# Performance work log

Hardware: AMD Instinct MI355X
Metric: run time of the kernel (lower is better)

## Reference

```python
import jax, jax.numpy as jnp
import numpy as np

N_NODES = 100000
N_EDGES = 6400000
D = 12

def setup_inputs() -> dict:
    key = jax.random.key(0)
    k1, k2, k3, k4 = jax.random.split(key, 4)
    x = jax.random.normal(k1, (N_NODES, D), dtype=jnp.float32)
    W_l = jax.random.normal(k2, (D, D), dtype=jnp.float32) / np.sqrt(D)
    W_r = jax.random.normal(k3, (D, D), dtype=jnp.float32) / np.sqrt(D)
    b = jnp.zeros((D,), dtype=jnp.float32)
    edge_index = jax.random.randint(k4, (2, N_EDGES), 0, N_NODES, dtype=jnp.int64)
    return {"x": x, "W_l": W_l, "W_r": W_r, "b": b, "edge_index": edge_index}

def reference(x, W_l, W_r, b, edge_index):
    # PyG SAGEConv (mean aggregation): out = lin_l(mean_{j in N(i)} x_j) + lin_r(x_i)
    src = edge_index[0]
    dst = edge_index[1]
    n = x.shape[0]
    msgs = x[src]                                      # [E, D] gather
    agg = jax.ops.segment_sum(msgs, dst, num_segments=n)          # [N, D]
    cnt = jax.ops.segment_sum(jnp.ones_like(dst, dtype=x.dtype), dst, num_segments=n)
    mean = agg / jnp.maximum(cnt, 1.0)[:, None]        # [N, D]
    out = mean @ W_l.T + x @ W_r.T + b                 # lin_l carries the bias in PyG
    return out
```

## Files before the change

kernel.cpp:

```cpp
#include <hip/hip_runtime.h>

#define N_NODES 100000
#define N_EDGES 6400000
#define D 12

#define SLOG 7
#define SSZ  128
#define NB   ((N_NODES + SSZ - 1) / SSZ)
#define NBLK 512
#define EPB  ((N_EDGES + NBLK - 1) / NBLK)
#define SBLK 256
#define STHR 512
#define SEPB ((N_EDGES + SBLK - 1) / SBLK)
#define RSTR 13

#define CAP  2048
#define EPT  (CAP / 256)

__device__ __forceinline__ unsigned int f2bf(float f) {
    unsigned int u = __float_as_uint(f);
    return (u + 0x7fffu + ((u >> 16) & 1u)) >> 16;
}
__device__ __forceinline__ unsigned int pk2(float lo, float hi) {
    return (f2bf(hi) << 16) | f2bf(lo);
}
__device__ __forceinline__ float bflo(unsigned int u) { return __uint_as_float(u << 16); }
__device__ __forceinline__ float bfhi(unsigned int u) { return __uint_as_float(u & 0xffff0000u); }

__global__ __launch_bounds__(256) void prep_kernel(
    const float* __restrict__ x, unsigned int* __restrict__ xb)
{
    int i = blockIdx.x * 256 + threadIdx.x;
    if (i >= N_NODES) return;
    const float4* xr = (const float4*)(x) + (size_t)i * 3;
    float4 a = xr[0], b = xr[1], c = xr[2];
    unsigned int* o = xb + (size_t)i * 8;
    ((uint4*)o)[0] = make_uint4(pk2(a.x, a.y), pk2(a.z, a.w), pk2(b.x, b.y), pk2(b.z, b.w));
    ((uint2*)(o + 4))[0] = make_uint2(pk2(c.x, c.y), pk2(c.z, c.w));
}

__global__ __launch_bounds__(256) void hist_kernel(
    const int* __restrict__ ei, int* __restrict__ bins)
{
    __shared__ int h[NB];
    for (int i = threadIdx.x; i < NB; i += 256) h[i] = 0;
    __syncthreads();
    const int* dei = ei + N_EDGES;
    int start = blockIdx.x * EPB;
    int end = min(start + EPB, N_EDGES);
    int e = start + (int)threadIdx.x;
    while (e + 768 < end) {
        int d0 = dei[e], d1 = dei[e + 256], d2 = dei[e + 512], d3 = dei[e + 768];
        atomicAdd(&h[d0 >> SLOG], 1);
        atomicAdd(&h[d1 >> SLOG], 1);
        atomicAdd(&h[d2 >> SLOG], 1);
        atomicAdd(&h[d3 >> SLOG], 1);
        e += 1024;
    }
    while (e < end) { atomicAdd(&h[dei[e] >> SLOG], 1); e += 256; }
    __syncthreads();
    for (int i = threadIdx.x; i < NB; i += 256) {
        int c = h[i];
        if (c) atomicAdd(&bins[i], c);
    }
}

__global__ __launch_bounds__(1024) void scan_kernel(
    const int* __restrict__ bins, int* __restrict__ base, int* __restrict__ cursor)
{
    __shared__ int buf[1024];
    __shared__ int carry;
    int tid = threadIdx.x;
    if (tid == 0) carry = 0;
    __syncthreads();
    for (int c0 = 0; c0 < NB; c0 += 1024) {
        int i = c0 + tid;
        int v = (i < NB) ? bins[i] : 0;
        buf[tid] = v;
        __syncthreads();
        for (int o = 1; o < 1024; o <<= 1) {
            int t = (tid >= o) ? buf[tid - o] : 0;
            __syncthreads();
            buf[tid] += t;
            __syncthreads();
        }
        int excl = buf[tid] - v + carry;
        if (i < NB) { base[i] = excl; cursor[i] = excl; }
        __syncthreads();
        if (tid == 0) carry += buf[1023];
        __syncthreads();
    }
    if (tid == 0) base[NB] = N_EDGES;
}

__global__ __launch_bounds__(512) void scatter_sort_kernel(
    const int* __restrict__ ei, int* __restrict__ cursor,
    unsigned int* __restrict__ sorted)
{
    __shared__ int h[NB];
    for (int i = threadIdx.x; i < NB; i += STHR) h[i] = 0;
    __syncthreads();
    const int* dei = ei + N_EDGES;
    int start = blockIdx.x * SEPB;
    int end = min(start + SEPB, N_EDGES);
    int e = start + (int)threadIdx.x;
    while (e + 3 * STHR < end) {
        int d0 = dei[e], d1 = dei[e + STHR], d2 = dei[e + 2 * STHR], d3 = dei[e + 3 * STHR];
        atomicAdd(&h[d0 >> SLOG], 1);
        atomicAdd(&h[d1 >> SLOG], 1);
        atomicAdd(&h[d2 >> SLOG], 1);
        atomicAdd(&h[d3 >> SLOG], 1);
        e += 4 * STHR;
    }
    while (e < end) { atomicAdd(&h[dei[e] >> SLOG], 1); e += STHR; }
    __syncthreads();
    for (int i = threadIdx.x; i < NB; i += STHR) {
        int c = h[i];
        h[i] = c ? atomicAdd(&cursor[i], c) : 0;
    }
    __syncthreads();
    e = start + (int)threadIdx.x;
    while (e + 3 * STHR < end) {
        int s0 = ei[e], s1 = ei[e + STHR], s2 = ei[e + 2 * STHR], s3 = ei[e + 3 * STHR];
        int d0 = dei[e], d1 = dei[e + STHR], d2 = dei[e + 2 * STHR], d3 = dei[e + 3 * STHR];
        int p0 = atomicAdd(&h[d0 >> SLOG], 1);
        int p1 = atomicAdd(&h[d1 >> SLOG], 1);
        int p2 = atomicAdd(&h[d2 >> SLOG], 1);
        int p3 = atomicAdd(&h[d3 >> SLOG], 1);
        sorted[p0] = ((unsigned)s0 << SLOG) | (unsigned)(d0 & (SSZ - 1));
        sorted[p1] = ((unsigned)s1 << SLOG) | (unsigned)(d1 & (SSZ - 1));
        sorted[p2] = ((unsigned)s2 << SLOG) | (unsigned)(d2 & (SSZ - 1));
        sorted[p3] = ((unsigned)s3 << SLOG) | (unsigned)(d3 & (SSZ - 1));
        e += 4 * STHR;
    }
    while (e < end) {
        int s = ei[e], d = dei[e];
        int pos = atomicAdd(&h[d >> SLOG], 1);
        sorted[pos] = ((unsigned)s << SLOG) | (unsigned)(d & (SSZ - 1));
        e += STHR;
    }
}

__global__ __launch_bounds__(256) void agg_reg_kernel(
    const unsigned int* __restrict__ sorted, const int* __restrict__ base,
    const unsigned int* __restrict__ xb,
    const float* __restrict__ x, const float* __restrict__ Wl,
    const float* __restrict__ Wr, const float* __restrict__ bias,
    float* __restrict__ out)
{
    __shared__ float sWl[D * D], sWr[D * D], sb[D];
    __shared__ int cnt[SSZ];
    __shared__ int sbuf[SSZ];
    __shared__ int segbase[SSZ + 1];
    __shared__ int cursor[SSZ];
    __shared__ int cnt_tot[SSZ];
    __shared__ unsigned vals[CAP * 6];

    int t = threadIdx.x;
    int b = blockIdx.x;

    if (t < D * D) { sWl[t] = Wl[t]; sWr[t] = Wr[t]; }
    if (t < D) sb[t] = bias[t];
    if (t < SSZ) cnt_tot[t] = 0;

    float acc[D];
#pragma unroll
    for (int d = 0; d < D; ++d) acc[d] = 0.f;

    int loc = t >> 1;
    int sub = t & 1;

    int start = base[b];
    int end = base[b + 1];

    for (int c0 = start; c0 < end; c0 += CAP) {
        int n = min(CAP, end - c0);
        if (t < SSZ) cnt[t] = 0;
        __syncthreads();

        unsigned pe[EPT];
        int ne = 0;
        for (int j = t; j < n; j += 256) pe[ne++] = sorted[c0 + j];
#pragma unroll
        for (int k = 0; k < EPT; ++k)
            if (k < ne) atomicAdd(&cnt[pe[k] & (SSZ - 1)], 1);
        __syncthreads();

        if (t < SSZ) sbuf[t] = cnt[t];
        __syncthreads();
        for (int o = 1; o < SSZ; o <<= 1) {
            int v = (t < SSZ && t >= o) ? sbuf[t - o] : 0;
            __syncthreads();
            if (t < SSZ) sbuf[t] += v;
            __syncthreads();
        }
        if (t < SSZ) {
            segbase[t + 1] = sbuf[t];
            if (t == 0) segbase[0] = 0;
        }
        __syncthreads();
        if (t < SSZ) { cursor[t] = segbase[t]; cnt_tot[t] += cnt[t]; }
        __syncthreads();

#pragma unroll
        for (int k = 0; k < EPT; ++k) {
            if (k < ne) {
                unsigned p = pe[k];
                int slot = atomicAdd(&cursor[p & (SSZ - 1)], 1);
                const unsigned* r = xb + (size_t)(p >> SLOG) * 8;
                uint2 q0 = ((const uint2*)r)[0];
                uint2 q1 = ((const uint2*)r)[1];
                uint2 q2 = ((const uint2*)r)[2];
                unsigned* vv = &vals[slot * 6];
                ((uint2*)vv)[0] = q0;
                ((uint2*)vv)[1] = q1;
                ((uint2*)vv)[2] = q2;
            }
        }
        __syncthreads();

        int s0 = segbase[loc], s1 = segbase[loc + 1];
        for (int j = s0 + sub; j < s1; j += 2) {
            const unsigned* vv = &vals[j * 6];
            uint2 q0 = ((const uint2*)vv)[0];
            uint2 q1 = ((const uint2*)vv)[1];
            uint2 q2 = ((const uint2*)vv)[2];
            acc[0]  += bflo(q0.x); acc[1]  += bfhi(q0.x);
            acc[2]  += bflo(q0.y); acc[3]  += bfhi(q0.y);
            acc[4]  += bflo(q1.x); acc[5]  += bfhi(q1.x);
            acc[6]  += bflo(q1.y); acc[7]  += bfhi(q1.y);
            acc[8]  += bflo(q2.x); acc[9]  += bfhi(q2.x);
            acc[10] += bflo(q2.y); acc[11] += bfhi(q2.y);
        }
        __syncthreads();
    }

    float* red = (float*)vals;
#pragma unroll
    for (int d = 0; d < D; ++d) red[sub * 1664 + loc * 13 + d] = acc[d];
    __syncthreads();

    if (t < SSZ) {
        int node = b * SSZ + t;
        if (node < N_NODES) {
            float m[D];
#pragma unroll
            for (int d = 0; d < D; ++d)
                m[d] = red[t * 13 + d] + red[1664 + t * 13 + d];
            float inv = 1.f / fmaxf((float)cnt_tot[t], 1.f);
#pragma unroll
            for (int d = 0; d < D; ++d) m[d] *= inv;

            float xi[D];
            const float4* xr = (const float4*)(x) + (size_t)node * 3;
            float4 x0 = xr[0], x1 = xr[1], x2 = xr[2];
            xi[0] = x0.x; xi[1] = x0.y; xi[2]  = x0.z; xi[3]  = x0.w;
            xi[4] = x1.x; xi[5] = x1.y; xi[6]  = x1.z; xi[7]  = x1.w;
            xi[8] = x2.x; xi[9] = x2.y; xi[10] = x2.z; xi[11] = x2.w;

            float o[D];
#pragma unroll
            for (int oo = 0; oo < D; ++oo) {
                float a = sb[oo];
#pragma unroll
                for (int d = 0; d < D; ++d) {
                    a += m[d] * sWl[oo * D + d];
                    a += xi[d] * sWr[oo * D + d];
                }
                o[oo] = a;
            }
            float4* orow = (float4*)(out) + (size_t)node * 3;
            orow[0] = make_float4(o[0], o[1], o[2], o[3]);
            orow[1] = make_float4(o[4], o[5], o[6], o[7]);
            orow[2] = make_float4(o[8], o[9], o[10], o[11]);
        }
    }
}

__global__ __launch_bounds__(256) void agg_finalize_f32_kernel(
    const unsigned int* __restrict__ sorted, const int* __restrict__ base,
    const float* __restrict__ x, const float* __restrict__ Wl,
    const float* __restrict__ Wr, const float* __restrict__ bias,
    float* __restrict__ out)
{
    __shared__ float agg[SSZ * RSTR];
    __shared__ float sWl[D * D], sWr[D * D], sb[D];
    int t = threadIdx.x;
    int b = blockIdx.x;
    for (int i = t; i < SSZ * RSTR; i += 256) agg[i] = 0.f;
    if (t < D * D) { sWl[t] = Wl[t]; sWr[t] = Wr[t]; }
    if (t < D) sb[t] = bias[t];
    __syncthreads();
    int start = base[b];
    int end = base[b + 1];
    for (int e = start + t; e < end; e += 256) {
        unsigned p = sorted[e];
        int src = (int)(p >> SLOG);
        int lc = (int)(p & (SSZ - 1));
        const float4* xr = (const float4*)(x) + (size_t)src * 3;
        float4 a = xr[0], b4 = xr[1], c = xr[2];
        float* ar = &agg[lc * RSTR];
        atomicAdd(ar + 0,  a.x);  atomicAdd(ar + 1,  a.y);
        atomicAdd(ar + 2,  a.z);  atomicAdd(ar + 3,  a.w);
        atomicAdd(ar + 4,  b4.x); atomicAdd(ar + 5,  b4.y);
        atomicAdd(ar + 6,  b4.z); atomicAdd(ar + 7,  b4.w);
        atomicAdd(ar + 8,  c.x);  atomicAdd(ar + 9,  c.y);
        atomicAdd(ar + 10, c.z);  atomicAdd(ar + 11, c.w);
        atomicAdd(ar + 12, 1.f);
    }
    __syncthreads();
    if (t < SSZ) {
        int node = b * SSZ + t;
        if (node < N_NODES) {
            const float* ar = &agg[t * RSTR];
            float inv = 1.f / fmaxf(ar[12], 1.f);
            float m[D], xi[D];
#pragma unroll
            for (int d = 0; d < D; ++d) m[d] = ar[d] * inv;
            const float4* xr = (const float4*)(x) + (size_t)node * 3;
            float4 x0 = xr[0], x1 = xr[1], x2 = xr[2];
            xi[0] = x0.x; xi[1] = x0.y; xi[2]  = x0.z; xi[3]  = x0.w;
            xi[4] = x1.x; xi[5] = x1.y; xi[6]  = x1.z; xi[7]  = x1.w;
            xi[8] = x2.x; xi[9] = x2.y; xi[10] = x2.z; xi[11] = x2.w;
            float o[D];
#pragma unroll
            for (int oo = 0; oo < D; ++oo) {
                float a = sb[oo];
#pragma unroll
                for (int d = 0; d < D; ++d) {
                    a += m[d] * sWl[oo * D + d];
                    a += xi[d] * sWr[oo * D + d];
                }
                o[oo] = a;
            }
            float4* orow = (float4*)(out) + (size_t)node * 3;
            orow[0] = make_float4(o[0], o[1], o[2], o[3]);
            orow[1] = make_float4(o[4], o[5], o[6], o[7]);
            orow[2] = make_float4(o[8], o[9], o[10], o[11]);
        }
    }
}


__global__ __launch_bounds__(256) void scatter_kernel(
    const int* __restrict__ ei, const float* __restrict__ x,
    float* __restrict__ agg, float* __restrict__ cnt)
{
    int e = blockIdx.x * blockDim.x + threadIdx.x;
    if (e >= N_EDGES) return;
    int src = ei[e];
    int dst = ei[N_EDGES + e];
    const float4* xr = (const float4*)(x + (size_t)src * D);
    float4 a = xr[0], b4 = xr[1], c = xr[2];
    float* dr = agg + (size_t)dst * D;
    atomicAdd(dr + 0,  a.x);  atomicAdd(dr + 1,  a.y);
    atomicAdd(dr + 2,  a.z);  atomicAdd(dr + 3,  a.w);
    atomicAdd(dr + 4,  b4.x); atomicAdd(dr + 5,  b4.y);
    atomicAdd(dr + 6,  b4.z); atomicAdd(dr + 7,  b4.w);
    atomicAdd(dr + 8,  c.x);  atomicAdd(dr + 9,  c.y);
    atomicAdd(dr + 10, c.z);  atomicAdd(dr + 11, c.w);
    atomicAdd(cnt + dst, 1.0f);
}

__global__ __launch_bounds__(256) void finalize_kernel(
    const float* __restrict__ x, const float* __restrict__ Wl,
    const float* __restrict__ Wr, const float* __restrict__ bias,
    const float* __restrict__ agg, const float* __restrict__ cnt,
    float* __restrict__ out)
{
    __shared__ float sWl[D * D], sWr[D * D], sb[D];
    int t = threadIdx.x;
    if (t < D * D) { sWl[t] = Wl[t]; sWr[t] = Wr[t]; }
    if (t < D) sb[t] = bias[t];
    __syncthreads();
    int i = blockIdx.x * blockDim.x + t;
    if (i >= N_NODES) return;
    float inv = 1.0f / fmaxf(cnt[i], 1.0f);
    float m[D], xi[D];
    const float4* ar = (const float4*)(agg + (size_t)i * D);
    const float4* xr = (const float4*)(x + (size_t)i * D);
    float4 a0 = ar[0], a1 = ar[1], a2 = ar[2];
    float4 x0 = xr[0], x1 = xr[1], x2 = xr[2];
    m[0] = a0.x * inv; m[1] = a0.y * inv; m[2]  = a0.z * inv; m[3]  = a0.w * inv;
    m[4] = a1.x * inv; m[5] = a1.y * inv; m[6]  = a1.z * inv; m[7]  = a1.w * inv;
    m[8] = a2.x * inv; m[9] = a2.y * inv; m[10] = a2.z * inv; m[11] = a2.w * inv;
    xi[0] = x0.x; xi[1] = x0.y; xi[2]  = x0.z; xi[3]  = x0.w;
    xi[4] = x1.x; xi[5] = x1.y; xi[6]  = x1.z; xi[7]  = x1.w;
    xi[8] = x2.x; xi[9] = x2.y; xi[10] = x2.z; xi[11] = x2.w;
    float o[D];
#pragma unroll
    for (int oo = 0; oo < D; ++oo) {
        float acc = sb[oo];
#pragma unroll
        for (int d = 0; d < D; ++d) {
            acc += m[d] * sWl[oo * D + d];
            acc += xi[d] * sWr[oo * D + d];
        }
        o[oo] = acc;
    }
    float4* orow = (float4*)(out + (size_t)i * D);
    orow[0] = make_float4(o[0], o[1], o[2], o[3]);
    orow[1] = make_float4(o[4], o[5], o[6], o[7]);
    orow[2] = make_float4(o[8], o[9], o[10], o[11]);
}

extern "C" void kernel_launch(void* const* d_in, const int* in_sizes, int n_in,
                              void* d_out, int out_size, void* d_ws, size_t ws_size,
                              hipStream_t stream) {
    const float* x    = (const float*)d_in[0];
    const float* Wl   = (const float*)d_in[1];
    const float* Wr   = (const float*)d_in[2];
    const float* bias = (const float*)d_in[3];
    const int*   ei   = (const int*)d_in[4];
    float* out = (float*)d_out;

    size_t sortedBytes = (size_t)N_EDGES * sizeof(unsigned int);
    size_t xbBytes     = (size_t)N_NODES * 8 * sizeof(unsigned int);
    size_t binsBytes   = (size_t)NB * sizeof(int);
    size_t baseBytes   = (size_t)(NB + 1) * sizeof(int);
    size_t neededFull = sortedBytes + xbBytes + binsBytes + baseBytes + binsBytes;
    size_t neededMid  = sortedBytes + binsBytes + baseBytes + binsBytes;
    size_t neededLast = ((size_t)N_NODES * D + N_NODES) * sizeof(float);

    if (ws_size >= neededFull) {
        char* p = (char*)d_ws;
        unsigned int* sorted = (unsigned int*)p;        p += sortedBytes;
        unsigned int* xb     = (unsigned int*)p;        p += xbBytes;
        int* bins   = (int*)p;                          p += binsBytes;
        int* base   = (int*)p;                          p += baseBytes;
        int* cursor = (int*)p;

        hipMemsetAsync(bins, 0, binsBytes, stream);
        prep_kernel<<<(N_NODES + 255) / 256, 256, 0, stream>>>(x, xb);
        hist_kernel<<<NBLK, 256, 0, stream>>>(ei, bins);
        scan_kernel<<<1, 1024, 0, stream>>>(bins, base, cursor);
        scatter_sort_kernel<<<SBLK, STHR, 0, stream>>>(ei, cursor, sorted);
        agg_reg_kernel<<<NB, 256, 0, stream>>>(sorted, base, xb, x, Wl, Wr, bias, out);
    } else if (ws_size >= neededMid) {
        char* p = (char*)d_ws;
        unsigned int* sorted = (unsigned int*)p;        p += sortedBytes;
        int* bins   = (int*)p;                          p += binsBytes;
        int* base   = (int*)p;                          p += baseBytes;
        int* cursor = (int*)p;

        hipMemsetAsync(bins, 0, binsBytes, stream);
        hist_kernel<<<NBLK, 256, 0, stream>>>(ei, bins);
        scan_kernel<<<1, 1024, 0, stream>>>(bins, base, cursor);
        scatter_sort_kernel<<<SBLK, STHR, 0, stream>>>(ei, cursor, sorted);
        agg_finalize_f32_kernel<<<NB, 256, 0, stream>>>(sorted, base, x, Wl, Wr, bias, out);
    } else {
        float* agg = (float*)d_ws;
        float* cnt = agg + (size_t)N_NODES * D;
        hipMemsetAsync(d_ws, 0, neededLast, stream);
        scatter_kernel<<<(N_EDGES + 255) / 256, 256, 0, stream>>>(ei, x, agg, cnt);
        finalize_kernel<<<(N_NODES + 255) / 256, 256, 0, stream>>>(x, Wl, Wr, bias, agg, cnt, out);
    }
}
```

Measured before the change: 271.8 us.

## Replace histogram+scan+sort with single-pass fixed-capacity strip scatter plus overflow buffer

Drops the separate histogram, scan and memset passes. A single scatter pass writes each edge into a fixed-capacity per-(bucket, block) strip, and edges that exceed the capacity go to a global overflow list. The aggregation kernel prefix-sums the strip lengths, processes the strips in chunks through shared memory, and then scans the overflow list for any matching edges. This saves a full read of the edge index and two launches. The cost is a larger, sparsely filled workspace and a serial overflow scan per block, which gets expensive if the degree distribution is skewed.

```diff
diff --git a/kernel.cpp b/kernel.cpp
--- a/kernel.cpp
+++ b/kernel.cpp
@@ -7,15 +7,19 @@
 #define SLOG 7
 #define SSZ  128
 #define NB   ((N_NODES + SSZ - 1) / SSZ)
+#define SBLK 256
+#define STHR 512
+#define SEPB (N_EDGES / SBLK)
+#define CAPS 64
+#define OVMAX 65536
+
+#define CAPE 1792
+#define SEGC 28
+
 #define NBLK 512
 #define EPB  ((N_EDGES + NBLK - 1) / NBLK)
-#define SBLK 256
-#define STHR 512
-#define SEPB ((N_EDGES + SBLK - 1) / SBLK)
-#define RSTR 13
-
-#define CAP  2048
-#define EPT  (CAP / 256)
+#define CAP4 2048
+#define EPT4 (CAP4 / 256)
 
 __device__ __forceinline__ unsigned int f2bf(float f) {
     unsigned int u = __float_as_uint(f);
@@ -28,9 +32,10 @@
 __device__ __forceinline__ float bfhi(unsigned int u) { return __uint_as_float(u & 0xffff0000u); }
 
 __global__ __launch_bounds__(256) void prep_kernel(
-    const float* __restrict__ x, unsigned int* __restrict__ xb)
+    const float* __restrict__ x, unsigned int* __restrict__ xb, int* ovctr)
 {
     int i = blockIdx.x * 256 + threadIdx.x;
+    if (i == 0 && ovctr) *ovctr = 0;
     if (i >= N_NODES) return;
     const float4* xr = (const float4*)(x) + (size_t)i * 3;
     float4 a = xr[0], b = xr[1], c = xr[2];
@@ -38,6 +43,233 @@
     ((uint4*)o)[0] = make_uint4(pk2(a.x, a.y), pk2(a.z, a.w), pk2(b.x, b.y), pk2(b.z, b.w));
     ((uint2*)(o + 4))[0] = make_uint2(pk2(c.x, c.y), pk2(c.z, c.w));
 }
+
+__global__ __launch_bounds__(512) void scatter1_kernel(
+    const int* __restrict__ ei, unsigned int* __restrict__ strip,
+    int* __restrict__ cnt, uint2* __restrict__ ovbuf, int* __restrict__ ovctr)
+{
+    __shared__ int cur[NB];
+    int t = threadIdx.x;
+    int b = blockIdx.x;
+    for (int i = t; i < NB; i += STHR) cur[i] = 0;
+    __syncthreads();
+
+    const int* dei = ei + N_EDGES;
+    int start = b * SEPB;
+    int end = start + SEPB;
+
+    int e = start + t;
+    while (e + 3 * STHR < end) {
+        int s0 = ei[e], s1 = ei[e + STHR], s2 = ei[e + 2 * STHR], s3 = ei[e + 3 * STHR];
+        int d0 = dei[e], d1 = dei[e + STHR], d2 = dei[e + 2 * STHR], d3 = dei[e + 3 * STHR];
+        int k0 = d0 >> SLOG, k1 = d1 >> SLOG, k2 = d2 >> SLOG, k3 = d3 >> SLOG;
+        int p0 = atomicAdd(&cur[k0], 1);
+        int p1 = atomicAdd(&cur[k1], 1);
+        int p2 = atomicAdd(&cur[k2], 1);
+        int p3 = atomicAdd(&cur[k3], 1);
+        if (p0 < CAPS) strip[((size_t)(k0 * SBLK + b)) * CAPS + p0] = ((unsigned)s0 << SLOG) | (unsigned)(d0 & (SSZ - 1));
+        else { int ix = atomicAdd(ovctr, 1); if (ix < OVMAX) ovbuf[ix] = make_uint2((unsigned)s0, (unsigned)d0); }
+        if (p1 < CAPS) strip[((size_t)(k1 * SBLK + b)) * CAPS + p1] = ((unsigned)s1 << SLOG) | (unsigned)(d1 & (SSZ - 1));
+        else { int ix = atomicAdd(ovctr, 1); if (ix < OVMAX) ovbuf[ix] = make_uint2((unsigned)s1, (unsigned)d1); }
+        if (p2 < CAPS) strip[((size_t)(k2 * SBLK + b)) * CAPS + p2] = ((unsigned)s2 << SLOG) | (unsigned)(d2 & (SSZ - 1));
+        else { int ix = atomicAdd(ovctr, 1); if (ix < OVMAX) ovbuf[ix] = make_uint2((unsigned)s2, (unsigned)d2); }
+        if (p3 < CAPS) strip[((size_t)(k3 * SBLK + b)) * CAPS + p3] = ((unsigned)s3 << SLOG) | (unsigned)(d3 & (SSZ - 1));
+        else { int ix = atomicAdd(ovctr, 1); if (ix < OVMAX) ovbuf[ix] = make_uint2((unsigned)s3, (unsigned)d3); }
+        e += 4 * STHR;
+    }
+    while (e < end) {
+        int s = ei[e], d = dei[e];
+        int k = d >> SLOG;
+        int p = atomicAdd(&cur[k], 1);
+        if (p < CAPS) strip[((size_t)(k * SBLK + b)) * CAPS + p] = ((unsigned)s << SLOG) | (unsigned)(d & (SSZ - 1));
+        else { int ix = atomicAdd(ovctr, 1); if (ix < OVMAX) ovbuf[ix] = make_uint2((unsigned)s, (unsigned)d); }
+        e += STHR;
+    }
+    __syncthreads();
+    int* crow = cnt + (size_t)b * NB;
+    for (int i = t; i < NB; i += STHR) crow[i] = cur[i];
+}
+
+__global__ __launch_bounds__(256) void agg_strip_kernel(
+    const unsigned int* __restrict__ strip, const int* __restrict__ cntm,
+    const uint2* __restrict__ ovbuf, const int* __restrict__ ovctr,
+    const unsigned int* __restrict__ xb,
+    const float* __restrict__ x, const float* __restrict__ Wl,
+    const float* __restrict__ Wr, const float* __restrict__ bias,
+    float* __restrict__ out)
+{
+    __shared__ float sWl[D * D], sWr[D * D], sb[D];
+    __shared__ int cnt[SSZ];
+    __shared__ int sbuf[SSZ];
+    __shared__ int segbase[SSZ + 1];
+    __shared__ int cursor[SSZ];
+    __shared__ int cnt_tot[SSZ];
+    __shared__ int seglen[SBLK];
+    __shared__ int segpre[SBLK + 1];
+    __shared__ unsigned vals[CAPE * 6];
+
+    int t = threadIdx.x;
+    int k = blockIdx.x;
+
+    if (t < D * D) { sWl[t] = Wl[t]; sWr[t] = Wr[t]; }
+    if (t < D) sb[t] = bias[t];
+    if (t < SSZ) cnt_tot[t] = 0;
+
+    if (t < SBLK) {
+        int c = cntm[(size_t)t * NB + k];
+        seglen[t] = c < CAPS ? c : CAPS;
+    }
+    __syncthreads();
+    if (t < SBLK) segpre[t + 1] = seglen[t];
+    if (t == 0) segpre[0] = 0;
+    __syncthreads();
+    for (int o = 1; o < SBLK; o <<= 1) {
+        int v = 0;
+        if (t < SBLK && t + 1 > o) v = segpre[t + 1 - o];
+        __syncthreads();
+        if (t < SBLK) segpre[t + 1] += v;
+        __syncthreads();
+    }
+
+    float acc[D];
+#pragma unroll
+    for (int d = 0; d < D; ++d) acc[d] = 0.f;
+
+    int loc = t >> 1;
+    int sub = t & 1;
+    int wave = t >> 6;
+    int lane = t & 63;
+
+    const unsigned int* kstrip = strip + (size_t)k * SBLK * CAPS;
+
+    for (int s0 = 0; s0 < SBLK; s0 += SEGC) {
+        int smax = s0 + SEGC < SBLK ? s0 + SEGC : SBLK;
+        int vbase = segpre[s0];
+        if (t < SSZ) cnt[t] = 0;
+        __syncthreads();
+
+        for (int s = s0 + wave; s < smax; s += 4) {
+            if (lane < seglen[s]) {
+                unsigned p = kstrip[(size_t)s * CAPS + lane];
+                atomicAdd(&cnt[p & (SSZ - 1)], 1);
+            }
+        }
+        __syncthreads();
+
+        if (t < SSZ) sbuf[t] = cnt[t];
+        __syncthreads();
+        for (int o = 1; o < SSZ; o <<= 1) {
+            int v = (t < SSZ && t >= o) ? sbuf[t - o] : 0;
+            __syncthreads();
+            if (t < SSZ) sbuf[t] += v;
+            __syncthreads();
+        }
+        if (t < SSZ) {
+            segbase[t + 1] = sbuf[t];
+            if (t == 0) segbase[0] = 0;
+        }
+        __syncthreads();
+        if (t < SSZ) { cursor[t] = segbase[t]; cnt_tot[t] += cnt[t]; }
+        __syncthreads();
+
+        for (int s = s0 + wave; s < smax; s += 4) {
+            if (lane < seglen[s]) {
+                unsigned p = kstrip[(size_t)s * CAPS + lane];
+                int slot = atomicAdd(&cursor[p & (SSZ - 1)], 1);
+                const unsigned* r = xb + (size_t)(p >> SLOG) * 8;
+                uint2 q0 = ((const uint2*)r)[0];
+                uint2 q1 = ((const uint2*)r)[1];
+                uint2 q2 = ((const uint2*)r)[2];
+                unsigned* vv = &vals[slot * 6];
+                ((uint2*)vv)[0] = q0;
+                ((uint2*)vv)[1] = q1;
+                ((uint2*)vv)[2] = q2;
+            }
+        }
+        __syncthreads();
+
+        int a0 = segbase[loc], a1 = segbase[loc + 1];
+        for (int j = a0 + sub; j < a1; j += 2) {
+            const unsigned* vv = &vals[j * 6];
+            uint2 q0 = ((const uint2*)vv)[0];
+            uint2 q1 = ((const uint2*)vv)[1];
+            uint2 q2 = ((const uint2*)vv)[2];
+            acc[0]  += bflo(q0.x); acc[1]  += bfhi(q0.x);
+            acc[2]  += bflo(q0.y); acc[3]  += bfhi(q0.y);
+            acc[4]  += bflo(q1.x); acc[5]  += bfhi(q1.x);
+            acc[6]  += bflo(q1.y); acc[7]  += bfhi(q1.y);
+            acc[8]  += bflo(q2.x); acc[9]  += bfhi(q2.x);
+            acc[10] += bflo(q2.y); acc[11] += bfhi(q2.y);
+        }
+        __syncthreads();
+        (void)vbase;
+    }
+
+    int novf = *ovctr;
+    if (novf > OVMAX) novf = OVMAX;
+    if (sub == 0 && novf > 0) {
+        int matches = 0;
+        for (int j = 0; j < novf; ++j) {
+            uint2 eo = ovbuf[j];
+            if ((int)(eo.y >> SLOG) == k && (int)(eo.y & (SSZ - 1)) == loc) {
+                const unsigned* r = xb + (size_t)eo.x * 8;
+                uint2 q0 = ((const uint2*)r)[0];
+                uint2 q1 = ((const uint2*)r)[1];
+                uint2 q2 = ((const uint2*)r)[2];
+                acc[0]  += bflo(q0.x); acc[1]  += bfhi(q0.x);
+                acc[2]  += bflo(q0.y); acc[3]  += bfhi(q0.y);
+                acc[4]  += bflo(q1.x); acc[5]  += bfhi(q1.x);
+                acc[6]  += bflo(q1.y); acc[7]  += bfhi(q1.y);
+                acc[8]  += bflo(q2.x); acc[9]  += bfhi(q2.x);
+                acc[10] += bflo(q2.y); acc[11] += bfhi(q2.y);
+                ++matches;
+            }
+        }
+        if (matches) atomicAdd(&cnt_tot[loc], matches);
+    }
+
+    float* red = (float*)vals;
+#pragma unroll
+    for (int d = 0; d < D; ++d) red[sub * 1664 + loc * 13 + d] = acc[d];
+    __syncthreads();
+
+    if (t < SSZ) {
+        int node = k * SSZ + t;
+        if (node < N_NODES) {
+            float m[D];
+#pragma unroll
+            for (int d = 0; d < D; ++d)
+                m[d] = red[t * 13 + d] + red[1664 + t * 13 + d];
+            float inv = 1.f / fmaxf((float)cnt_tot[t], 1.f);
+#pragma unroll
+            for (int d = 0; d < D; ++d) m[d] *= inv;
+
+            float xi[D];
+            const float4* xr = (const float4*)(x) + (size_t)node * 3;
+            float4 x0 = xr[0], x1 = xr[1], x2 = xr[2];
+            xi[0] = x0.x; xi[1] = x0.y; xi[2]  = x0.z; xi[3]  = x0.w;
+            xi[4] = x1.x; xi[5] = x1.y; xi[6]  = x1.z; xi[7]  = x1.w;
+            xi[8] = x2.x; xi[9] = x2.y; xi[10] = x2.z; xi[11] = x2.w;
+
+            float o[D];
+#pragma unroll
+            for (int oo = 0; oo < D; ++oo) {
+                float a = sb[oo];
+#pragma unroll
+                for (int d = 0; d < D; ++d) {
+                    a += m[d] * sWl[oo * D + d];
+                    a += xi[d] * sWr[oo * D + d];
+                }
+                o[oo] = a;
+            }
+            float4* orow = (float4*)(out) + (size_t)node * 3;
+            orow[0] = make_float4(o[0], o[1], o[2], o[3]);
+            orow[1] = make_float4(o[4], o[5], o[6], o[7]);
+            orow[2] = make_float4(o[8], o[9], o[10], o[11]);
+        }
+    }
+}
+
 
 __global__ __launch_bounds__(256) void hist_kernel(
     const int* __restrict__ ei, int* __restrict__ bins)
@@ -141,7 +373,7 @@
     }
 }
 
-__global__ __launch_bounds__(256) void agg_reg_kernel(
+__global__ __launch_bounds__(256) void agg_reg4_kernel(
     const unsigned int* __restrict__ sorted, const int* __restrict__ base,
     const unsigned int* __restrict__ xb,
     const float* __restrict__ x, const float* __restrict__ Wl,
@@ -154,7 +386,7 @@
     __shared__ int segbase[SSZ + 1];
     __shared__ int cursor[SSZ];
     __shared__ int cnt_tot[SSZ];
-    __shared__ unsigned vals[CAP * 6];
+    __shared__ unsigned vals[CAP4 * 6];
 
     int t = threadIdx.x;
     int b = blockIdx.x;
@@ -173,17 +405,17 @@
     int start = base[b];
     int end = base[b + 1];
 
-    for (int c0 = start; c0 < end; c0 += CAP) {
-        int n = min(CAP, end - c0);
+    for (int c0 = start; c0 < end; c0 += CAP4) {
+        int n = min(CAP4, end - c0);
         if (t < SSZ) cnt[t] = 0;
         __syncthreads();
 
-        unsigned pe[EPT];
+        unsigned pe[EPT4];
         int ne = 0;
         for (int j = t; j < n; j += 256) pe[ne++] = sorted[c0 + j];
 #pragma unroll
-        for (int k = 0; k < EPT; ++k)
-            if (k < ne) atomicAdd(&cnt[pe[k] & (SSZ - 1)], 1);
+        for (int q = 0; q < EPT4; ++q)
+            if (q < ne) atomicAdd(&cnt[pe[q] & (SSZ - 1)], 1);
         __syncthreads();
 
         if (t < SSZ) sbuf[t] = cnt[t];
@@ -203,9 +435,9 @@
         __syncthreads();
 
 #pragma unroll
-        for (int k = 0; k < EPT; ++k) {
-            if (k < ne) {
-                unsigned p = pe[k];
+        for (int q = 0; q < EPT4; ++q) {
+            if (q < ne) {
+                unsigned p = pe[q];
                 int slot = atomicAdd(&cursor[p & (SSZ - 1)], 1);
                 const unsigned* r = xb + (size_t)(p >> SLOG) * 8;
                 uint2 q0 = ((const uint2*)r)[0];
@@ -219,8 +451,8 @@
         }
         __syncthreads();
 
-        int s0 = segbase[loc], s1 = segbase[loc + 1];
-        for (int j = s0 + sub; j < s1; j += 2) {
+        int a0 = segbase[loc], a1 = segbase[loc + 1];
+        for (int j = a0 + sub; j < a1; j += 2) {
             const unsigned* vv = &vals[j * 6];
             uint2 q0 = ((const uint2*)vv)[0];
             uint2 q1 = ((const uint2*)vv)[1];
@@ -258,70 +490,6 @@
             xi[4] = x1.x; xi[5] = x1.y; xi[6]  = x1.z; xi[7]  = x1.w;
             xi[8] = x2.x; xi[9] = x2.y; xi[10] = x2.z; xi[11] = x2.w;
 
-            float o[D];
-#pragma unroll
-            for (int oo = 0; oo < D; ++oo) {
-                float a = sb[oo];
-#pragma unroll
-                for (int d = 0; d < D; ++d) {
-                    a += m[d] * sWl[oo * D + d];
-                    a += xi[d] * sWr[oo * D + d];
-                }
-                o[oo] = a;
-            }
-            float4* orow = (float4*)(out) + (size_t)node * 3;
-            orow[0] = make_float4(o[0], o[1], o[2], o[3]);
-            orow[1] = make_float4(o[4], o[5], o[6], o[7]);
-            orow[2] = make_float4(o[8], o[9], o[10], o[11]);
-        }
-    }
-}
-
-__global__ __launch_bounds__(256) void agg_finalize_f32_kernel(
-    const unsigned int* __restrict__ sorted, const int* __restrict__ base,
-    const float* __restrict__ x, const float* __restrict__ Wl,
-    const float* __restrict__ Wr, const float* __restrict__ bias,
-    float* __restrict__ out)
-{
-    __shared__ float agg[SSZ * RSTR];
-    __shared__ float sWl[D * D], sWr[D * D], sb[D];
-    int t = threadIdx.x;
-    int b = blockIdx.x;
-    for (int i = t; i < SSZ * RSTR; i += 256) agg[i] = 0.f;
-    if (t < D * D) { sWl[t] = Wl[t]; sWr[t] = Wr[t]; }
-    if (t < D) sb[t] = bias[t];
-    __syncthreads();
-    int start = base[b];
-    int end = base[b + 1];
-    for (int e = start + t; e < end; e += 256) {
-        unsigned p = sorted[e];
-        int src = (int)(p >> SLOG);
-        int lc = (int)(p & (SSZ - 1));
-        const float4* xr = (const float4*)(x) + (size_t)src * 3;
-        float4 a = xr[0], b4 = xr[1], c = xr[2];
-        float* ar = &agg[lc * RSTR];
-        atomicAdd(ar + 0,  a.x);  atomicAdd(ar + 1,  a.y);
-        atomicAdd(ar + 2,  a.z);  atomicAdd(ar + 3,  a.w);
-        atomicAdd(ar + 4,  b4.x); atomicAdd(ar + 5,  b4.y);
-        atomicAdd(ar + 6,  b4.z); atomicAdd(ar + 7,  b4.w);
-        atomicAdd(ar + 8,  c.x);  atomicAdd(ar + 9,  c.y);
-        atomicAdd(ar + 10, c.z);  atomicAdd(ar + 11, c.w);
-        atomicAdd(ar + 12, 1.f);
-    }
-    __syncthreads();
-    if (t < SSZ) {
-        int node = b * SSZ + t;
-        if (node < N_NODES) {
-            const float* ar = &agg[t * RSTR];
-            float inv = 1.f / fmaxf(ar[12], 1.f);
-            float m[D], xi[D];
-#pragma unroll
-            for (int d = 0; d < D; ++d) m[d] = ar[d] * inv;
-            const float4* xr = (const float4*)(x) + (size_t)node * 3;
-            float4 x0 = xr[0], x1 = xr[1], x2 = xr[2];
-            xi[0] = x0.x; xi[1] = x0.y; xi[2]  = x0.z; xi[3]  = x0.w;
-            xi[4] = x1.x; xi[5] = x1.y; xi[6]  = x1.z; xi[7]  = x1.w;
-            xi[8] = x2.x; xi[9] = x2.y; xi[10] = x2.z; xi[11] = x2.w;
             float o[D];
 #pragma unroll
             for (int oo = 0; oo < D; ++oo) {
@@ -414,15 +582,30 @@
     const int*   ei   = (const int*)d_in[4];
     float* out = (float*)d_out;
 
+    size_t stripBytes  = (size_t)NB * SBLK * CAPS * sizeof(unsigned int);
+    size_t xbBytes     = (size_t)N_NODES * 8 * sizeof(unsigned int);
+    size_t cntBytes    = (size_t)SBLK * NB * sizeof(int);
+    size_t ovBytes     = (size_t)OVMAX * sizeof(uint2);
+    size_t neededNew   = stripBytes + xbBytes + cntBytes + ovBytes + 64;
+
     size_t sortedBytes = (size_t)N_EDGES * sizeof(unsigned int);
-    size_t xbBytes     = (size_t)N_NODES * 8 * sizeof(unsigned int);
     size_t binsBytes   = (size_t)NB * sizeof(int);
     size_t baseBytes   = (size_t)(NB + 1) * sizeof(int);
-    size_t neededFull = sortedBytes + xbBytes + binsBytes + baseBytes + binsBytes;
-    size_t neededMid  = sortedBytes + binsBytes + baseBytes + binsBytes;
-    size_t neededLast = ((size_t)N_NODES * D + N_NODES) * sizeof(float);
-
-    if (ws_size >= neededFull) {
+    size_t neededMid   = sortedBytes + xbBytes + binsBytes + baseBytes + binsBytes;
+    size_t neededLast  = ((size_t)N_NODES * D + N_NODES) * sizeof(float);
+
+    if (ws_size >= neededNew) {
+        char* p = (char*)d_ws;
+        unsigned int* strip = (unsigned int*)p;         p += stripBytes;
+        unsigned int* xb    = (unsigned int*)p;         p += xbBytes;
+        int* cnt    = (int*)p;                          p += cntBytes;
+        uint2* ovbuf = (uint2*)p;                       p += ovBytes;
+        int* ovctr  = (int*)p;
+
+        prep_kernel<<<(N_NODES + 255) / 256, 256, 0, stream>>>(x, xb, ovctr);
+        scatter1_kernel<<<SBLK, STHR, 0, stream>>>(ei, strip, cnt, ovbuf, ovctr);
+        agg_strip_kernel<<<NB, 256, 0, stream>>>(strip, cnt, ovbuf, ovctr, xb, x, Wl, Wr, bias, out);
+    } else if (ws_size >= neededMid) {
         char* p = (char*)d_ws;
         unsigned int* sorted = (unsigned int*)p;        p += sortedBytes;
         unsigned int* xb     = (unsigned int*)p;        p += xbBytes;
@@ -431,23 +614,11 @@
         int* cursor = (int*)p;
 
         hipMemsetAsync(bins, 0, binsBytes, stream);
-        prep_kernel<<<(N_NODES + 255) / 256, 256, 0, stream>>>(x, xb);
+        prep_kernel<<<(N_NODES + 255) / 256, 256, 0, stream>>>(x, xb, nullptr);
         hist_kernel<<<NBLK, 256, 0, stream>>>(ei, bins);
         scan_kernel<<<1, 1024, 0, stream>>>(bins, base, cursor);
         scatter_sort_kernel<<<SBLK, STHR, 0, stream>>>(ei, cursor, sorted);
-        agg_reg_kernel<<<NB, 256, 0, stream>>>(sorted, base, xb, x, Wl, Wr, bias, out);
-    } else if (ws_size >= neededMid) {
-        char* p = (char*)d_ws;
-        unsigned int* sorted = (unsigned int*)p;        p += sortedBytes;
-        int* bins   = (int*)p;                          p += binsBytes;
-        int* base   = (int*)p;                          p += baseBytes;
-        int* cursor = (int*)p;
-
-        hipMemsetAsync(bins, 0, binsBytes, stream);
-        hist_kernel<<<NBLK, 256, 0, stream>>>(ei, bins);
-        scan_kernel<<<1, 1024, 0, stream>>>(bins, base, cursor);
-        scatter_sort_kernel<<<SBLK, STHR, 0, stream>>>(ei, cursor, sorted);
-        agg_finalize_f32_kernel<<<NB, 256, 0, stream>>>(sorted, base, x, Wl, Wr, bias, out);
+        agg_reg4_kernel<<<NB, 256, 0, stream>>>(sorted, base, xb, x, Wl, Wr, bias, out);
     } else {
         float* agg = (float*)d_ws;
         float* cnt = agg + (size_t)N_NODES * D;
```

Measured after the change: 328.9 us. 21.0% more time.
